# Kernel tuning notes

Measured on AMD Instinct MI355X. Metric: run time of the kernel, lower is better.

## Reference

```python
import jax, jax.numpy as jnp
import numpy as np

_SAMPLING_EPS = 1e-5
B, V = 256, 128000


def _apply_min_p(logits, min_p):
    # probs >= min_p * max_prob  <=>  keep; else logit -> -inf
    probs = jax.nn.softmax(logits, axis=-1)
    max_probs = jnp.max(probs, axis=-1, keepdims=True)
    keep = probs >= (min_p[:, None] * max_probs)
    return jnp.where(keep, logits, -jnp.inf)


def _apply_top_k_top_p(logits, top_k, top_p):
    # Sort ascending once; derive per-row keep-thresholds for both filters.
    logits_sort = jnp.sort(logits, axis=-1)  # [B, V] ascending
    # top-k threshold: value at position V-k (kth largest)
    k_idx = jnp.clip(V - top_k, 0, V - 1).astype(jnp.int32)
    k_thresh = jnp.take_along_axis(logits_sort, k_idx[:, None], axis=-1)  # [B,1]
    # top-p: on ascending-sorted probs, token is kept iff cumsum > 1 - p
    probs_sort = jax.nn.softmax(logits_sort, axis=-1)
    probs_cum = jnp.cumsum(probs_sort, axis=-1)
    kept = probs_cum > (1.0 - top_p[:, None])
    kept = kept.at[:, -1].set(True)  # always keep the max-prob token
    p_thresh = jnp.min(jnp.where(kept, logits_sort, jnp.inf), axis=-1, keepdims=True)
    thresh = jnp.maximum(k_thresh, p_thresh)
    return jnp.where(logits >= thresh, logits, -jnp.inf)


def setup_inputs() -> dict:
    key = jax.random.key(0)
    k1, k2, k3, k4, k5 = jax.random.split(key, 5)
    logits = jax.random.normal(k1, (B, V), jnp.float32)
    temperature = jax.random.uniform(k2, (B,), jnp.float32, 0.1, 1.5)
    temperature = temperature.at[:8].set(0.0)  # greedy rows
    min_p = jax.random.uniform(k3, (B,), jnp.float32, 0.0, 0.2)
    top_k = jax.random.randint(k4, (B,), 1, 64).astype(jnp.int32)
    top_p = jax.random.uniform(k5, (B,), jnp.float32, 0.5, 1.0)
    return {"logits": logits, "temperature": temperature, "min_p": min_p,
            "top_k": top_k, "top_p": top_p}


def reference(logits, temperature, min_p, top_k, top_p):
    logits = logits.astype(jnp.float32)
    greedy = jnp.argmax(logits, axis=-1)  # [B]
    # safe temperature divide (greedy rows have temp ~ 0 but are overridden)
    safe_t = jnp.where(temperature < _SAMPLING_EPS, 1.0, temperature)
    scaled = logits / safe_t[:, None]
    scaled = _apply_min_p(scaled, min_p)
    masked = _apply_top_k_top_p(scaled, top_k, top_p)
    # Gumbel-max trick == categorical sampling from softmax(masked)
    u = jax.random.uniform(jax.random.key(42), masked.shape, jnp.float32, 1e-10, 1.0)
    gumbel = -jnp.log(-jnp.log(u))
    random_sampled = jnp.argmax(masked + gumbel, axis=-1)
    sampled = jnp.where(temperature < _SAMPLING_EPS, greedy, random_sampled)
    return sampled[:, None]  # sampled_token_ids [B, 1]
```

## Files before the change

### kernel.cpp

```cpp
#include <hip/hip_runtime.h>
#include <stdint.h>

typedef unsigned long long u64;
typedef unsigned int u32;

#define VOCAB 128000
#define NV4   32000
#define NROWS 256
#define BLK   1024
#define NW    16
#define NB    4096
#define CAPL  4096
#define SEPS  1e-5f
#define LN2X40 27.725887222397812f

__device__ __forceinline__ u32 f2key(float f){
  u32 u = __float_as_uint(f);
  return (u & 0x80000000u) ? ~u : (u | 0x80000000u);
}
__device__ __forceinline__ float key2f(u32 k){
  u32 u = (k & 0x80000000u) ? (k ^ 0x80000000u) : ~k;
  return __uint_as_float(u);
}

__device__ __forceinline__ void tf2x32(u32 x0, u32 x1, u32 &o0, u32 &o1){
  const u32 k0 = 0u, k1 = 42u, k2 = 0u ^ 42u ^ 0x1BD11BDAu;
  x0 += k0; x1 += k1;
#define TFR(r) { x0 += x1; x1 = (x1 << (r)) | (x1 >> (32 - (r))); x1 ^= x0; }
  TFR(13) TFR(15) TFR(26) TFR(6)
  x0 += k1; x1 += k2 + 1u;
  TFR(17) TFR(29) TFR(16) TFR(24)
  x0 += k2; x1 += k0 + 2u;
  TFR(13) TFR(15) TFR(26) TFR(6)
  x0 += k0; x1 += k1 + 3u;
  TFR(17) TFR(29) TFR(16) TFR(24)
  x0 += k1; x1 += k2 + 4u;
  TFR(13) TFR(15) TFR(26) TFR(6)
  x0 += k2; x1 += k0 + 5u;
#undef TFR
  o0 = x0; o1 = x1;
}
__device__ __forceinline__ u32 gumbel_bits(u32 i){
  u32 o0, o1; tf2x32(0u, i, o0, o1);
  return o0 ^ o1;
}
__device__ __forceinline__ float bits2gumbel(u32 b){
  float f = __uint_as_float(0x3F800000u | (b >> 9)) - 1.0f;
  float u = fmaxf(1e-10f, f + 1e-10f);
  return -logf(-logf(u));
}

__device__ __forceinline__ void cross4096_u32(
    const u32* arr, u32* aux, u32 target, u32* out_idx, u32* out_before, int t)
{
  aux[t] = arr[4*t+0] + arr[4*t+1] + arr[4*t+2] + arr[4*t+3];
  __syncthreads();
  if (t < 64){
    u32 gs = 0u;
    #pragma unroll
    for (int j=0;j<16;j++) gs += aux[t*16+j];
    u32 pref = gs;
    #pragma unroll
    for (int d=1; d<64; d<<=1){ u32 v = __shfl_up(pref, d, 64); if (t >= d) pref += v; }
    u64 bal = __ballot(pref > target);
    int g = bal ? (__ffsll((long long)bal) - 1) : 63;
    u32 pg = __shfl(pref, g, 64);
    u32 gg = __shfl(gs, g, 64);
    if (t == 0){
      u32 c = pg - gg;
      u32 idx = (u32)(g*64 + 63);
      for (int j=0;j<16;j++){
        u32 v = aux[g*16+j];
        if (c + v > target){
          int base = (g*16+j)*4;
          for (int q=0;q<4;q++){
            u32 w = arr[base+q];
            if (c + w > target){ idx = (u32)(base+q); goto doneu; }
            c += w;
          }
        }
        c += v;
      }
      doneu:
      *out_idx = idx; *out_before = c;
    }
  }
}

__device__ __forceinline__ void cross4096_u64(
    const u64* arr, u64* aux, u64 target, u32* out_idx, u64* out_before, int t)
{
  aux[t] = arr[4*t+0] + arr[4*t+1] + arr[4*t+2] + arr[4*t+3];
  __syncthreads();
  if (t < 64){
    u64 gs = 0ull;
    #pragma unroll
    for (int j=0;j<16;j++) gs += aux[t*16+j];
    u64 pref = gs;
    #pragma unroll
    for (int d=1; d<64; d<<=1){
      u64 v = __shfl_up((unsigned long long)pref, d, 64); if (t >= d) pref += v;
    }
    u64 bal = __ballot(pref > target);
    int g = bal ? (__ffsll((long long)bal) - 1) : 63;
    u64 pg = __shfl((unsigned long long)pref, g, 64);
    u64 gg = __shfl((unsigned long long)gs, g, 64);
    if (t == 0){
      u64 c = pg - gg;
      u32 idx = (u32)(g*64 + 63);
      for (int j=0;j<16;j++){
        u64 v = aux[g*16+j];
        if (c + v > target){
          int base = (g*16+j)*4;
          for (int q=0;q<4;q++){
            u64 w = arr[base+q];
            if (c + w > target){ idx = (u32)(base+q); goto donev; }
            c += w;
          }
        }
        c += v;
      }
      donev:
      *out_idx = idx; *out_before = c;
    }
  }
}

__device__ __forceinline__ void cross4096_mass(
    const u64* arr, u64* aux, float topp_v, u64* out_target,
    u32* out_idx, u64* out_before, int t)
{
  aux[t] = arr[4*t+0] + arr[4*t+1] + arr[4*t+2] + arr[4*t+3];
  __syncthreads();
  if (t < 64){
    u64 gs = 0ull;
    #pragma unroll
    for (int j=0;j<16;j++) gs += aux[t*16+j];
    u64 pref = gs;
    #pragma unroll
    for (int d=1; d<64; d<<=1){
      u64 v = __shfl_up((unsigned long long)pref, d, 64); if (t >= d) pref += v;
    }
    u64 total = __shfl((unsigned long long)pref, 63, 64);
    u64 target = (u64)((double)(1.0f - topp_v) * (double)total);
    u64 bal = __ballot(pref > target);
    int g = bal ? (__ffsll((long long)bal) - 1) : 63;
    u64 pg = __shfl((unsigned long long)pref, g, 64);
    u64 gg = __shfl((unsigned long long)gs, g, 64);
    if (t == 0){
      u64 c = pg - gg;
      u32 idx = (u32)(g*64 + 63);
      for (int j=0;j<16;j++){
        u64 v = aux[g*16+j];
        if (c + v > target){
          int base = (g*16+j)*4;
          for (int q=0;q<4;q++){
            u64 w = arr[base+q];
            if (c + w > target){ idx = (u32)(base+q); goto donem; }
            c += w;
          }
        }
        c += v;
      }
      donem:
      *out_target = target; *out_idx = idx; *out_before = c;
    }
  }
}

__device__ __forceinline__ void cross256_u32(const u32* arr, u32 target, u32* out_idx, int t){
  if (t < 64){
    u32 gs = arr[4*t+0]+arr[4*t+1]+arr[4*t+2]+arr[4*t+3];
    u32 pref = gs;
    #pragma unroll
    for (int d=1; d<64; d<<=1){ u32 v=__shfl_up(pref,d,64); if (t>=d) pref+=v; }
    u64 bal = __ballot(pref > target);
    int g = bal ? (__ffsll((long long)bal)-1) : 63;
    u32 pg=__shfl(pref,g,64), gg=__shfl(gs,g,64);
    if (t==0){
      u32 c = pg-gg; u32 idx=(u32)(g*4+3);
      for (int q=0;q<4;q++){ u32 w=arr[g*4+q]; if (c+w>target){ idx=(u32)(g*4+q); break; } c+=w; }
      *out_idx = idx;
    }
  }
}
__device__ __forceinline__ void cross256_u64(const u64* arr, u64 target, u32* out_idx, int t){
  if (t < 64){
    u64 gs = arr[4*t+0]+arr[4*t+1]+arr[4*t+2]+arr[4*t+3];
    u64 pref = gs;
    #pragma unroll
    for (int d=1; d<64; d<<=1){
      u64 v=__shfl_up((unsigned long long)pref,d,64); if (t>=d) pref+=v;
    }
    u64 bal = __ballot(pref > target);
    int g = bal ? (__ffsll((long long)bal)-1) : 63;
    u64 pg=__shfl((unsigned long long)pref,g,64), gg=__shfl((unsigned long long)gs,g,64);
    if (t==0){
      u64 c = pg-gg; u32 idx=(u32)(g*4+3);
      for (int q=0;q<4;q++){ u64 w=arr[g*4+q]; if (c+w>target){ idx=(u32)(g*4+q); break; } c+=w; }
      *out_idx = idx;
    }
  }
}

__device__ __forceinline__ void msmerge(float &m1, float &S1, float m2, float S2){
  float mm = fmaxf(m1, m2);
  if (mm == -INFINITY){ m1 = mm; S1 = 0.0f; return; }
  S1 = S1*__expf(m1-mm) + S2*__expf(m2-mm);
  m1 = mm;
}

__device__ __forceinline__ void argmax_write(
    float best, u32 bi, float* wrf, u32* wru, int ln, int wv, int b, int* out)
{
  #pragma unroll
  for (int d=32; d>0; d>>=1){
    float c2=__shfl_down(best,d,64); u32 i2=__shfl_down(bi,d,64);
    if (c2>best || (c2==best && i2<bi)){best=c2;bi=i2;}
  }
  if (ln==0){ wrf[wv]=best; wru[wv]=bi; }
  __syncthreads();
  if (wv==0){
    float b1=(ln<NW)?wrf[ln]:-INFINITY; u32 i1=(ln<NW)?wru[ln]:0xFFFFFFFFu;
    #pragma unroll
    for (int d=32; d>0; d>>=1){
      float b2=__shfl_down(b1,d,64); u32 i2=__shfl_down(i1,d,64);
      if (b2>b1 || (b2==b1 && i2<i1)){b1=b2;i1=i2;}
    }
    if (ln==0) out[b]=(int)i1;
  }
}

__global__ __launch_bounds__(BLK) void k_all(
    const float* __restrict__ logits, const float* __restrict__ temp,
    const float* __restrict__ minp, const int* __restrict__ topk,
    const float* __restrict__ topp, int* __restrict__ out)
{
  __shared__ u32 cnt[NB];
  __shared__ u64 massI[2*NB];
  __shared__ u64 list[CAPL];
  __shared__ u64 aux64[BLK];
  __shared__ float wrf1[NW], wrf2[NW];
  __shared__ u32  wru1[NW], wru2[NW];
  __shared__ float sh_m, sh_Z;
  __shared__ u32 sh_lstar, sh_len, sh_idx, sh_bef32, sh_u1, sh_u2, sh_u3;
  __shared__ u64 sh_bef64, sh_tfix;

  u32* aux32 = (u32*)aux64;

  const int b = blockIdx.x;
  const int t = threadIdx.x;
  const int ln = t & 63, wv = t >> 6;
  const float T = temp[b];
  const float* row = logits + (size_t)b * VOCAB;
  const float4* row4 = (const float4*)row;

  if (T < SEPS){
    float M = -INFINITY; u32 Mi = 0xFFFFFFFFu;
    for (int i=t; i<NV4; i+=BLK){
      float4 q = row4[i];
      #pragma unroll
      for (int j=0;j<4;j++){
        float l = (&q.x)[j]; u32 gi = (u32)(i*4+j);
        if (l > M){ M = l; Mi = gi; }
      }
    }
    argmax_write(M, Mi, wrf1, wru1, ln, wv, b, out);
    return;
  }

  const float invT = 1.0f / T;
  for (int i=t;i<NB;i+=BLK) cnt[i]=0u;
  for (int i=t;i<2*NB;i+=BLK) massI[i]=0ull;
  if (t==0) sh_len=0u;
  __syncthreads();

  float ms0=-INFINITY,S0=0.0f, ms1=-INFINITY,S1=0.0f,
        ms2=-INFINITY,S2=0.0f, ms3=-INFINITY,S3=0.0f;
#define ONLINE(LV, MS, SS) { \
    float l_ = (LV); \
    atomicAdd(&cnt[f2key(l_)>>20], 1u); \
    float s_ = l_ * invT; \
    float d_ = s_ - MS; \
    float e_ = __expf(-fabsf(d_)); \
    if (d_ > 0.0f){ SS = fmaf(SS, e_, 1.0f); MS = s_; } else { SS += e_; } \
  }
  for (int i=t; i<NV4; i+=2*BLK){
    float4 qa = row4[i];
    int i2 = i + BLK; bool h2 = (i2 < NV4);
    float4 qb; if (h2) qb = row4[i2];
    ONLINE(qa.x,ms0,S0) ONLINE(qa.y,ms1,S1) ONLINE(qa.z,ms2,S2) ONLINE(qa.w,ms3,S3)
    if (h2){
      ONLINE(qb.x,ms0,S0) ONLINE(qb.y,ms1,S1) ONLINE(qb.z,ms2,S2) ONLINE(qb.w,ms3,S3)
    }
  }
#undef ONLINE
  msmerge(ms0,S0,ms1,S1); msmerge(ms2,S2,ms3,S3); msmerge(ms0,S0,ms2,S2);
  #pragma unroll
  for (int d=32; d>0; d>>=1){
    float mz = __shfl_down(ms0, d, 64); float Sz = __shfl_down(S0, d, 64);
    msmerge(ms0, S0, mz, Sz);
  }
  if (ln==0){ wrf1[wv]=ms0; wrf2[wv]=S0; }
  __syncthreads();
  if (wv==0){
    float m1 = (ln<NW)? wrf1[ln] : -INFINITY;
    float Sx = (ln<NW)? wrf2[ln] : 0.0f;
    #pragma unroll
    for (int d=32; d>0; d>>=1){
      float mz=__shfl_down(m1,d,64); float Sz=__shfl_down(Sx,d,64);
      msmerge(m1, Sx, mz, Sz);
    }
    if (ln==0){ sh_m = m1; sh_Z = Sx; }
  }
  __syncthreads();
  const float m = sh_m, Z = sh_Z;

  int tk = topk[b]; if (tk < 1) tk = 1; if (tk > VOCAB) tk = VOCAB;
  cross4096_u32(cnt, aux32, (u32)(VOCAB - tk), &sh_idx, &sh_bef32, t);
  __syncthreads();
  const u32 b1k = sh_idx;
  const u32 r1  = (u32)(VOCAB - tk + 1) - sh_bef32;

  if (wv==0){
    const float rhs = minp[b] * (1.0f / Z);
    u32 lo = 0u, hi = 0xFF800000u;
    while (hi - lo > 64u){
      u32 step = (hi - lo) >> 6;
      u32 k = lo + (u32)(ln + 1) * step;
      float e = __expf(fmaf(key2f(k), invT, -m));
      u64 bal = __ballot((e / Z) >= rhs);
      if (bal){
        u32 g = (u32)(__ffsll((long long)bal) - 1);
        hi = lo + (g + 1u) * step;
        lo = lo + g * step;
      } else {
        lo += 64u * step;
      }
    }
    u32 k = lo + 1u + (u32)ln;
    bool ok = (k <= hi);
    float e = __expf(fmaf(key2f(k), invT, -m));
    u64 bal = __ballot(ok && ((e / Z) >= rhs));
    if (ln==0) sh_lstar = bal ? (lo + 1u + (u32)(__ffsll((long long)bal) - 1)) : hi;
  }
  __syncthreads();
  const u32 lstar = sh_lstar;
  const u32 bl = lstar >> 20;

  {
    u32 pa=0u, pc=0u;
    for (int i=t;i<NB;i+=BLK){
      u32 c = cnt[i];
      if ((u32)i > bl)   pa += c;
      if ((u32)i >= b1k) pc += c;
    }
    #pragma unroll
    for (int d=32; d>0; d>>=1){ pa += __shfl_down(pa,d,64); pc += __shfl_down(pc,d,64); }
    if (ln==0){ wru1[wv]=pa; wru2[wv]=pc; }
    __syncthreads();
    if (t==0){
      u32 a=0u, c2=0u;
      for (int w=0; w<NW; w++){ a += wru1[w]; c2 += wru2[w]; }
      sh_u1 = a; sh_u2 = c2;
    }
    __syncthreads();
  }
  const u32 Kmin = sh_u1;
  const bool kcert = (Kmin >= (u32)tk);
  const u32 CLB = kcert ? b1k : bl;
  const u32 listlen = kcert ? sh_u2 : (Kmin + cnt[bl]);
  const bool fastOK = (listlen <= (u32)CAPL);
  const float cs = LN2X40 - m;

  u32 kc = 0u;
#define P2E(LV, IDX) { \
    float l_ = (LV); u32 key_ = f2key(l_); u32 bk_ = key_ >> 20; \
    if (key_ >= lstar){ \
      kc++; \
      u64 lm_ = (u64)__expf(fmaf(l_, invT, cs)); \
      if (lm_) atomicAdd(&massI[(bk_<<1) | (u32)(t&1)], lm_); \
    } \
    if (fastOK && bk_ >= CLB){ \
      u32 p_ = atomicAdd(&sh_len, 1u); \
      if (p_ < CAPL) list[p_] = ((u64)key_ << 32) | (u64)(u32)(IDX); \
    } \
  }
  for (int i=t; i<NV4; i+=2*BLK){
    float4 qa = row4[i];
    int i2 = i + BLK; bool h2 = (i2 < NV4);
    float4 qb; if (h2) qb = row4[i2];
    P2E(qa.x, i*4+0) P2E(qa.y, i*4+1) P2E(qa.z, i*4+2) P2E(qa.w, i*4+3)
    if (h2){
      P2E(qb.x, i2*4+0) P2E(qb.y, i2*4+1) P2E(qb.z, i2*4+2) P2E(qb.w, i2*4+3)
    }
  }
#undef P2E
  #pragma unroll
  for (int d=32; d>0; d>>=1) kc += __shfl_down(kc, d, 64);
  if (ln==0) wru1[wv] = kc;
  __syncthreads();
  if (t==0){ u32 K2=0u; for (int w=0;w<NW;w++) K2 += wru1[w]; sh_u3 = K2; }
  {
    u64 g0 = massI[8*t+0] + massI[8*t+1];
    u64 g1 = massI[8*t+2] + massI[8*t+3];
    u64 g2 = massI[8*t+4] + massI[8*t+5];
    u64 g3 = massI[8*t+6] + massI[8*t+7];
    __syncthreads();
    massI[4*t+0]=g0; massI[4*t+1]=g1; massI[4*t+2]=g2; massI[4*t+3]=g3;
  }
  __syncthreads();
  const u32 K = sh_u3;
  const bool kval = (K >= (u32)tk);
  const u32 llen = sh_len;

  cross4096_mass(massI, aux64, topp[b], &sh_tfix, &sh_idx, &sh_bef64, t);
  __syncthreads();
  const u32 b1p = sh_idx;
  const u64 t1  = sh_tfix - sh_bef64;
  const bool needK = kval && (b1p <= b1k);
  const bool needP = (!kval) || (b1p >= b1k);

  u32 kkey = 0u, pkey = 0u;

  if (fastOK){
    if (needK){
      for (int i=t;i<NB;i+=BLK) cnt[i]=0u;
      __syncthreads();
      for (u32 i=t; i<llen; i+=BLK){
        u32 key = (u32)(list[i]>>32);
        if ((key>>20) == b1k) atomicAdd(&cnt[(key>>8)&0xFFFu], 1u);
      }
      __syncthreads();
      cross4096_u32(cnt, aux32, r1-1u, &sh_idx, &sh_bef32, t);
      __syncthreads();
      u32 b2k = sh_idx, r2 = r1 - sh_bef32;
      u32 prefk = (b1k<<12) | b2k;
      for (int i=t;i<256;i+=BLK) cnt[i]=0u;
      __syncthreads();
      for (u32 i=t; i<llen; i+=BLK){
        u32 key = (u32)(list[i]>>32);
        if ((key>>8) == prefk) atomicAdd(&cnt[key&0xFFu], 1u);
      }
      __syncthreads();
      cross256_u32(cnt, r2-1u, &sh_idx, t);
      __syncthreads();
      kkey = (prefk<<8) | sh_idx;
    }
    if (needP){
      for (int i=t;i<NB;i+=BLK) massI[i]=0ull;
      __syncthreads();
      for (u32 i=t; i<llen; i+=BLK){
        u32 key = (u32)(list[i]>>32);
        if ((key>>20) == b1p && key >= lstar){
          u64 lm = (u64)__expf(fmaf(key2f(key), invT, cs));
          if (lm) atomicAdd(&massI[(key>>8)&0xFFFu], lm);
        }
      }
      __syncthreads();
      cross4096_u64(massI, aux64, t1, &sh_idx, &sh_bef64, t);
      __syncthreads();
      u32 b2p = sh_idx; u64 t2 = t1 - sh_bef64;
      u32 prefp = (b1p<<12) | b2p;
      for (int i=t;i<256;i+=BLK) massI[i]=0ull;
      __syncthreads();
      for (u32 i=t; i<llen; i+=BLK){
        u32 key = (u32)(list[i]>>32);
        if ((key>>8) == prefp && key >= lstar){
          u64 lm = (u64)__expf(fmaf(key2f(key), invT, cs));
          if (lm) atomicAdd(&massI[key&0xFFu], lm);
        }
      }
      __syncthreads();
      cross256_u64(massI, t2, &sh_idx, t);
      __syncthreads();
      pkey = (prefp<<8) | sh_idx;
    }
    const u32 thrkey = kkey > pkey ? kkey : pkey;

    float best = -INFINITY; u32 bi = 0xFFFFFFFFu;
    for (u32 i=t; i<llen; i+=BLK){
      u64 e = list[i];
      u32 key = (u32)(e>>32);
      if (key >= thrkey){
        u32 idx = (u32)e;
        u32 c = (u32)b * (u32)VOCAB + idx;
        float cand = key2f(key)*invT + bits2gumbel(gumbel_bits(c));
        if (cand > best || (cand == best && idx < bi)){ best = cand; bi = idx; }
      }
    }
    argmax_write(best, bi, wrf1, wru1, ln, wv, b, out);
    return;
  }

  for (int i=t;i<NB;i+=BLK){ cnt[i]=0u; massI[i]=0ull; }
  __syncthreads();
  for (int i=t; i<NV4; i+=BLK){
    float4 q = row4[i];
    #pragma unroll
    for (int j=0;j<4;j++){
      float l = (&q.x)[j]; u32 key = f2key(l); u32 hb = key>>20;
      if (needK && hb == b1k) atomicAdd(&cnt[(key>>8)&0xFFFu], 1u);
      if (needP && hb == b1p && key >= lstar){
        u64 lm = (u64)__expf(fmaf(l, invT, cs));
        if (lm) atomicAdd(&massI[(key>>8)&0xFFFu], lm);
      }
    }
  }
  __syncthreads();
  u32 b2k = 0u, r2 = 1u, b2p = 0u; u64 t2 = 0ull;
  if (needK){
    cross4096_u32(cnt, aux32, r1-1u, &sh_idx, &sh_bef32, t);
    __syncthreads();
    b2k = sh_idx; r2 = r1 - sh_bef32;
  }
  if (needP){
    cross4096_u64(massI, aux64, t1, &sh_idx, &sh_bef64, t);
    __syncthreads();
    b2p = sh_idx; t2 = t1 - sh_bef64;
  }
  const u32 prefk = (b1k<<12) | b2k;
  const u32 prefp = (b1p<<12) | b2p;
  for (int i=t;i<256;i+=BLK){ cnt[i]=0u; massI[i]=0ull; }
  __syncthreads();
  for (int i=t; i<NV4; i+=BLK){
    float4 q = row4[i];
    #pragma unroll
    for (int j=0;j<4;j++){
      float l = (&q.x)[j]; u32 key = f2key(l);
      if (needK && (key>>8) == prefk) atomicAdd(&cnt[key&0xFFu], 1u);
      if (needP && (key>>8) == prefp && key >= lstar){
        u64 lm = (u64)__expf(fmaf(l, invT, cs));
        if (lm) atomicAdd(&massI[key&0xFFu], lm);
      }
    }
  }
  __syncthreads();
  if (needK){
    cross256_u32(cnt, r2-1u, &sh_idx, t);
    __syncthreads();
    kkey = (prefk<<8) | sh_idx;
  }
  if (needP){
    cross256_u64(massI, t2, &sh_idx, t);
    __syncthreads();
    pkey = (prefp<<8) | sh_idx;
  }
  const float thrf = key2f(kkey > pkey ? kkey : pkey);
  float best = -INFINITY; u32 bi = 0xFFFFFFFFu;
  for (int i=t; i<NV4; i+=BLK){
    float4 q = row4[i];
    #pragma unroll
    for (int j=0;j<4;j++){
      float l = (&q.x)[j];
      if (l >= thrf){
        u32 idx = (u32)(i*4+j);
        u32 c = (u32)b * (u32)VOCAB + idx;
        float cand = l*invT + bits2gumbel(gumbel_bits(c));
        if (cand > best || (cand == best && idx < bi)){ best = cand; bi = idx; }
      }
    }
  }
  argmax_write(best, bi, wrf1, wru1, ln, wv, b, out);
}

extern "C" void kernel_launch(void* const* d_in, const int* in_sizes, int n_in,
                              void* d_out, int out_size, void* d_ws, size_t ws_size,
                              hipStream_t stream)
{
  const float* logits = (const float*)d_in[0];
  const float* temp   = (const float*)d_in[1];
  const float* minp   = (const float*)d_in[2];
  const int*   topk   = (const int*)d_in[3];
  const float* topp   = (const float*)d_in[4];
  int* out = (int*)d_out;

  hipLaunchKernelGGL(k_all, dim3(NROWS), dim3(BLK), 0, stream,
                     logits, temp, minp, topk, topp, out);
}
```

Baseline: 60.18 us.

## Privatize histograms per wave group, aggregate list appends, and unroll row loops

```diff
diff --git a/kernel.cpp b/kernel.cpp
--- a/kernel.cpp
+++ b/kernel.cpp
@@ -13,6 +13,7 @@
 #define CAPL  4096
 #define SEPS  1e-5f
 #define LN2X40 27.725887222397812f
+#define MAIN4 28672
 
 __device__ __forceinline__ u32 f2key(float f){
   u32 u = __float_as_uint(f);
@@ -236,8 +237,8 @@
     const float* __restrict__ minp, const int* __restrict__ topk,
     const float* __restrict__ topp, int* __restrict__ out)
 {
-  __shared__ u32 cnt[NB];
-  __shared__ u64 massI[2*NB];
+  __shared__ u32 cnt4[4*NB];
+  __shared__ u64 massI[NB];
   __shared__ u64 list[CAPL];
   __shared__ u64 aux64[BLK];
   __shared__ float wrf1[NW], wrf2[NW];
@@ -247,6 +248,7 @@
   __shared__ u64 sh_bef64, sh_tfix;
 
   u32* aux32 = (u32*)aux64;
+  u32* cnt = cnt4;
 
   const int b = blockIdx.x;
   const int t = threadIdx.x;
@@ -257,42 +259,51 @@
 
   if (T < SEPS){
     float M = -INFINITY; u32 Mi = 0xFFFFFFFFu;
-    for (int i=t; i<NV4; i+=BLK){
-      float4 q = row4[i];
-      #pragma unroll
-      for (int j=0;j<4;j++){
-        float l = (&q.x)[j]; u32 gi = (u32)(i*4+j);
-        if (l > M){ M = l; Mi = gi; }
-      }
-    }
+#define GRE(Q, IDX) { \
+    float l_=(Q); if (l_ > M){ M = l_; Mi = (u32)(IDX); } }
+    for (int i=t; i<MAIN4; i+=4096){
+      float4 q0=row4[i], q1=row4[i+1024], q2=row4[i+2048], q3=row4[i+3072];
+      GRE(q0.x,i*4+0) GRE(q0.y,i*4+1) GRE(q0.z,i*4+2) GRE(q0.w,i*4+3)
+      GRE(q1.x,(i+1024)*4+0) GRE(q1.y,(i+1024)*4+1) GRE(q1.z,(i+1024)*4+2) GRE(q1.w,(i+1024)*4+3)
+      GRE(q2.x,(i+2048)*4+0) GRE(q2.y,(i+2048)*4+1) GRE(q2.z,(i+2048)*4+2) GRE(q2.w,(i+2048)*4+3)
+      GRE(q3.x,(i+3072)*4+0) GRE(q3.y,(i+3072)*4+1) GRE(q3.z,(i+3072)*4+2) GRE(q3.w,(i+3072)*4+3)
+    }
+    for (int i=MAIN4+t; i<NV4; i+=BLK){
+      float4 q=row4[i];
+      GRE(q.x,i*4+0) GRE(q.y,i*4+1) GRE(q.z,i*4+2) GRE(q.w,i*4+3)
+    }
+#undef GRE
     argmax_write(M, Mi, wrf1, wru1, ln, wv, b, out);
     return;
   }
 
   const float invT = 1.0f / T;
-  for (int i=t;i<NB;i+=BLK) cnt[i]=0u;
-  for (int i=t;i<2*NB;i+=BLK) massI[i]=0ull;
+  for (int i=t;i<4*NB;i+=BLK) cnt4[i]=0u;
+  for (int i=t;i<NB;i+=BLK) massI[i]=0ull;
   if (t==0) sh_len=0u;
   __syncthreads();
 
+  u32* mycnt = cnt4 + (((u32)wv & 3u) << 12);
   float ms0=-INFINITY,S0=0.0f, ms1=-INFINITY,S1=0.0f,
         ms2=-INFINITY,S2=0.0f, ms3=-INFINITY,S3=0.0f;
 #define ONLINE(LV, MS, SS) { \
     float l_ = (LV); \
-    atomicAdd(&cnt[f2key(l_)>>20], 1u); \
+    atomicAdd(&mycnt[f2key(l_)>>20], 1u); \
     float s_ = l_ * invT; \
     float d_ = s_ - MS; \
     float e_ = __expf(-fabsf(d_)); \
     if (d_ > 0.0f){ SS = fmaf(SS, e_, 1.0f); MS = s_; } else { SS += e_; } \
   }
-  for (int i=t; i<NV4; i+=2*BLK){
-    float4 qa = row4[i];
-    int i2 = i + BLK; bool h2 = (i2 < NV4);
-    float4 qb; if (h2) qb = row4[i2];
-    ONLINE(qa.x,ms0,S0) ONLINE(qa.y,ms1,S1) ONLINE(qa.z,ms2,S2) ONLINE(qa.w,ms3,S3)
-    if (h2){
-      ONLINE(qb.x,ms0,S0) ONLINE(qb.y,ms1,S1) ONLINE(qb.z,ms2,S2) ONLINE(qb.w,ms3,S3)
-    }
+  for (int i=t; i<MAIN4; i+=4096){
+    float4 q0=row4[i], q1=row4[i+1024], q2=row4[i+2048], q3=row4[i+3072];
+    ONLINE(q0.x,ms0,S0) ONLINE(q0.y,ms1,S1) ONLINE(q0.z,ms2,S2) ONLINE(q0.w,ms3,S3)
+    ONLINE(q1.x,ms0,S0) ONLINE(q1.y,ms1,S1) ONLINE(q1.z,ms2,S2) ONLINE(q1.w,ms3,S3)
+    ONLINE(q2.x,ms0,S0) ONLINE(q2.y,ms1,S1) ONLINE(q2.z,ms2,S2) ONLINE(q2.w,ms3,S3)
+    ONLINE(q3.x,ms0,S0) ONLINE(q3.y,ms1,S1) ONLINE(q3.z,ms2,S2) ONLINE(q3.w,ms3,S3)
+  }
+  for (int i=MAIN4+t; i<NV4; i+=BLK){
+    float4 q=row4[i];
+    ONLINE(q.x,ms0,S0) ONLINE(q.y,ms1,S1) ONLINE(q.z,ms2,S2) ONLINE(q.w,ms3,S3)
   }
 #undef ONLINE
   msmerge(ms0,S0,ms1,S1); msmerge(ms2,S2,ms3,S3); msmerge(ms0,S0,ms2,S2);
@@ -303,6 +314,10 @@
   }
   if (ln==0){ wrf1[wv]=ms0; wrf2[wv]=S0; }
   __syncthreads();
+  for (int i=t; i<NB; i+=BLK){
+    u32 s = cnt4[i] + cnt4[NB+i] + cnt4[2*NB+i] + cnt4[3*NB+i];
+    cnt4[i] = s;
+  }
   if (wv==0){
     float m1 = (ln<NW)? wrf1[ln] : -INFINITY;
     float Sx = (ln<NW)? wrf2[ln] : 0.0f;
@@ -375,25 +390,33 @@
 
   u32 kc = 0u;
 #define P2E(LV, IDX) { \
-    float l_ = (LV); u32 key_ = f2key(l_); u32 bk_ = key_ >> 20; \
+    float l_ = (LV); u32 key_ = f2key(l_); \
     if (key_ >= lstar){ \
       kc++; \
       u64 lm_ = (u64)__expf(fmaf(l_, invT, cs)); \
-      if (lm_) atomicAdd(&massI[(bk_<<1) | (u32)(t&1)], lm_); \
+      if (lm_) atomicAdd(&massI[key_>>20], lm_); \
     } \
-    if (fastOK && bk_ >= CLB){ \
-      u32 p_ = atomicAdd(&sh_len, 1u); \
+    bool cand_ = fastOK && ((key_>>20) >= CLB); \
+    u64 bal_ = __ballot(cand_); \
+    if (cand_){ \
+      u32 lead_ = (u32)__ffsll((long long)bal_) - 1u; \
+      u32 base_ = 0u; \
+      if ((u32)ln == lead_) base_ = atomicAdd(&sh_len, (u32)__popcll(bal_)); \
+      base_ = __shfl(base_, (int)lead_, 64); \
+      u32 p_ = base_ + (u32)__popcll(bal_ & ((1ull << ln) - 1ull)); \
       if (p_ < CAPL) list[p_] = ((u64)key_ << 32) | (u64)(u32)(IDX); \
     } \
   }
-  for (int i=t; i<NV4; i+=2*BLK){
-    float4 qa = row4[i];
-    int i2 = i + BLK; bool h2 = (i2 < NV4);
-    float4 qb; if (h2) qb = row4[i2];
-    P2E(qa.x, i*4+0) P2E(qa.y, i*4+1) P2E(qa.z, i*4+2) P2E(qa.w, i*4+3)
-    if (h2){
-      P2E(qb.x, i2*4+0) P2E(qb.y, i2*4+1) P2E(qb.z, i2*4+2) P2E(qb.w, i2*4+3)
-    }
+  for (int i=t; i<MAIN4; i+=4096){
+    float4 q0=row4[i], q1=row4[i+1024], q2=row4[i+2048], q3=row4[i+3072];
+    P2E(q0.x,i*4+0) P2E(q0.y,i*4+1) P2E(q0.z,i*4+2) P2E(q0.w,i*4+3)
+    P2E(q1.x,(i+1024)*4+0) P2E(q1.y,(i+1024)*4+1) P2E(q1.z,(i+1024)*4+2) P2E(q1.w,(i+1024)*4+3)
+    P2E(q2.x,(i+2048)*4+0) P2E(q2.y,(i+2048)*4+1) P2E(q2.z,(i+2048)*4+2) P2E(q2.w,(i+2048)*4+3)
+    P2E(q3.x,(i+3072)*4+0) P2E(q3.y,(i+3072)*4+1) P2E(q3.z,(i+3072)*4+2) P2E(q3.w,(i+3072)*4+3)
+  }
+  for (int i=MAIN4+t; i<NV4; i+=BLK){
+    float4 q=row4[i];
+    P2E(q.x,i*4+0) P2E(q.y,i*4+1) P2E(q.z,i*4+2) P2E(q.w,i*4+3)
   }
 #undef P2E
   #pragma unroll
@@ -401,14 +424,6 @@
   if (ln==0) wru1[wv] = kc;
   __syncthreads();
   if (t==0){ u32 K2=0u; for (int w=0;w<NW;w++) K2 += wru1[w]; sh_u3 = K2; }
-  {
-    u64 g0 = massI[8*t+0] + massI[8*t+1];
-    u64 g1 = massI[8*t+2] + massI[8*t+3];
-    u64 g2 = massI[8*t+4] + massI[8*t+5];
-    u64 g3 = massI[8*t+6] + massI[8*t+7];
-    __syncthreads();
-    massI[4*t+0]=g0; massI[4*t+1]=g1; massI[4*t+2]=g2; massI[4*t+3]=g3;
-  }
   __syncthreads();
   const u32 K = sh_u3;
   const bool kval = (K >= (u32)tk);
```

Result: no change. 61.18 us (+1.7%).

## Split each row across two cooperative blocks with grid-synchronized merge

Applied to the files above, without the earlier changes.

```diff
diff --git a/kernel.cpp b/kernel.cpp
--- a/kernel.cpp
+++ b/kernel.cpp
@@ -1,18 +1,34 @@
 #include <hip/hip_runtime.h>
+#include <hip/hip_cooperative_groups.h>
 #include <stdint.h>
+
+namespace cg = cooperative_groups;
 
 typedef unsigned long long u64;
 typedef unsigned int u32;
 
 #define VOCAB 128000
 #define NV4   32000
+#define HV4   16000
 #define NROWS 256
 #define BLK   1024
 #define NW    16
 #define NB    4096
-#define CAPL  4096
+#define CAPL  2048
+#define CAPLS 4096
 #define SEPS  1e-5f
 #define LN2X40 27.725887222397812f
+
+#define WS_MASSH   0ull
+#define WS_LIST    16777216ull
+#define WS_CNTH    20971520ull
+#define WS_PARTS   29360128ull
+#define WS_PARTK   29362176ull
+#define WS_PARTGV  29364224ull
+#define WS_PARTGI  29366272ull
+#define WS_LL      29368320ull
+#define WS_KP      29369344ull
+#define WS_NEED    29370368ull
 
 __device__ __forceinline__ u32 f2key(float f){
   u32 u = __float_as_uint(f);
@@ -231,14 +247,400 @@
   }
 }
 
-__global__ __launch_bounds__(BLK) void k_all(
+__global__ __launch_bounds__(BLK, 8) void k_coop(
+    const float* __restrict__ logits, const float* __restrict__ temp,
+    const float* __restrict__ minp, const int* __restrict__ topk,
+    const float* __restrict__ topp, int* __restrict__ out, char* __restrict__ ws)
+{
+  cg::grid_group grid = cg::this_grid();
+
+  __shared__ u32 cnt[NB];
+  __shared__ u64 massI[NB];
+  __shared__ u64 list[CAPL];
+  __shared__ u64 aux64[BLK];
+  __shared__ float wrf1[NW];
+  __shared__ u32  wru1[NW], wru2[NW];
+  __shared__ u32 sh_idx, sh_bef32, sh_lstar, sh_u1, sh_u2;
+  __shared__ u64 sh_bef64, sh_tfix;
+
+  u32* aux32 = (u32*)aux64;
+  u64* massH  = (u64*)(ws + WS_MASSH);
+  u64* wsList = (u64*)(ws + WS_LIST);
+  u32* cntH   = (u32*)(ws + WS_CNTH);
+  float* partS  = (float*)(ws + WS_PARTS);
+  u32*   partK  = (u32*)(ws + WS_PARTK);
+  float* partGV = (float*)(ws + WS_PARTGV);
+  u32*   partGI = (u32*)(ws + WS_PARTGI);
+  u32*   LL     = (u32*)(ws + WS_LL);
+  u32*   KP     = (u32*)(ws + WS_KP);
+
+  const int bid = blockIdx.x;
+  const int r = bid >> 1;
+  const int h = bid & 1;
+  const int t = threadIdx.x;
+  const int ln = t & 63, wv = t >> 6;
+  const float T = temp[r];
+  const bool greedy = (T < SEPS);
+  const float invT = greedy ? 1.0f : (1.0f / T);
+  const float* row = logits + (size_t)r * VOCAB;
+  const float4* row4 = (const float4*)row;
+  const int hb4 = h * HV4, he4 = hb4 + HV4;
+
+  if (t == 0 && h == 0){ LL[r] = 0u; KP[r] = 0u; }
+  if (greedy){
+    float M = -INFINITY; u32 Mi = 0xFFFFFFFFu;
+    for (int i = hb4 + t; i < he4; i += BLK){
+      float4 q = row4[i];
+      #pragma unroll
+      for (int j=0;j<4;j++){
+        float l = (&q.x)[j]; u32 gi = (u32)(i*4+j);
+        if (l > M){ M = l; Mi = gi; }
+      }
+    }
+    #pragma unroll
+    for (int d=32; d>0; d>>=1){
+      float M2=__shfl_down(M,d,64); u32 I2=__shfl_down(Mi,d,64);
+      if (M2>M || (M2==M && I2<Mi)){ M=M2; Mi=I2; }
+    }
+    if (ln==0){ wrf1[wv]=M; wru1[wv]=Mi; }
+    __syncthreads();
+    if (t==0){
+      float b1=wrf1[0]; u32 i1=wru1[0];
+      for (int w=1; w<NW; w++){
+        if (wrf1[w]>b1 || (wrf1[w]==b1 && wru1[w]<i1)){ b1=wrf1[w]; i1=wru1[w]; }
+      }
+      partGV[bid]=b1; partGI[bid]=i1;
+    }
+  } else {
+    for (int i=t;i<NB;i+=BLK) cnt[i]=0u;
+    __syncthreads();
+    u32 km = 0u;
+    float S0=0.0f,S1=0.0f,S2=0.0f,S3=0.0f;
+#define PA(LV, SS) { \
+    float l_=(LV); u32 k_=f2key(l_); \
+    if (k_>km) km=k_; \
+    atomicAdd(&cnt[k_>>20], 1u); \
+    SS += __expf(l_*invT); }
+    for (int i = hb4 + t; i < he4; i += 2*BLK){
+      float4 qa = row4[i];
+      int i2 = i + BLK; bool h2 = (i2 < he4);
+      float4 qb; if (h2) qb = row4[i2];
+      PA(qa.x,S0) PA(qa.y,S1) PA(qa.z,S2) PA(qa.w,S3)
+      if (h2){ PA(qb.x,S0) PA(qb.y,S1) PA(qb.z,S2) PA(qb.w,S3) }
+    }
+#undef PA
+    float S = (S0+S1)+(S2+S3);
+    #pragma unroll
+    for (int d=32; d>0; d>>=1){
+      S += __shfl_down(S,d,64);
+      u32 k2 = __shfl_down(km,d,64); if (k2>km) km=k2;
+    }
+    if (ln==0){ wrf1[wv]=S; wru1[wv]=km; }
+    __syncthreads();
+    for (int i=t;i<NB;i+=BLK) cntH[(size_t)bid*NB + i] = cnt[i];
+    if (t==0){
+      float St=0.0f; u32 kt=0u;
+      for (int w=0; w<NW; w++){ St += wrf1[w]; if (wru1[w]>kt) kt=wru1[w]; }
+      partS[bid]=St; partK[bid]=kt;
+    }
+  }
+  __threadfence();
+  grid.sync();
+
+  float m=0.0f, Z=1.0f, cs=0.0f;
+  u32 b1k=0u, r1=1u, lstar=0u, CLB=0u;
+  int tk=1; bool kcert=false, fastOK=false;
+
+  if (greedy){
+    if (h==0 && t==0){
+      float vA=partGV[bid], vB=partGV[bid+1];
+      u32 iA=partGI[bid], iB=partGI[bid+1];
+      out[r] = (vB>vA || (vB==vA && iB<iA)) ? (int)iB : (int)iA;
+    }
+  } else {
+    const int pb = bid ^ 1;
+    for (int i=t;i<NB;i+=BLK) cnt[i] += cntH[(size_t)pb*NB + i];
+    {
+      u32 kA = partK[bid & ~1], kB = partK[bid | 1];
+      float SA = partS[bid & ~1], SB = partS[bid | 1];
+      u32 kmax = kA > kB ? kA : kB;
+      m = key2f(kmax) * invT;
+      Z = (SA + SB) * __expf(-m);
+    }
+    cs = LN2X40 - m;
+    __syncthreads();
+
+    tk = topk[r]; if (tk < 1) tk = 1; if (tk > VOCAB) tk = VOCAB;
+    cross4096_u32(cnt, aux32, (u32)(VOCAB - tk), &sh_idx, &sh_bef32, t);
+    __syncthreads();
+    b1k = sh_idx;
+    r1  = (u32)(VOCAB - tk + 1) - sh_bef32;
+
+    if (wv==0){
+      const float rhs = minp[r] * (1.0f / Z);
+      u32 lo = 0u, hi = 0xFF800000u;
+      while (hi - lo > 64u){
+        u32 step = (hi - lo) >> 6;
+        u32 k = lo + (u32)(ln + 1) * step;
+        float e = __expf(fmaf(key2f(k), invT, -m));
+        u64 bal = __ballot((e / Z) >= rhs);
+        if (bal){
+          u32 g = (u32)(__ffsll((long long)bal) - 1);
+          hi = lo + (g + 1u) * step;
+          lo = lo + g * step;
+        } else {
+          lo += 64u * step;
+        }
+      }
+      u32 k = lo + 1u + (u32)ln;
+      bool ok = (k <= hi);
+      float e = __expf(fmaf(key2f(k), invT, -m));
+      u64 bal = __ballot(ok && ((e / Z) >= rhs));
+      if (ln==0) sh_lstar = bal ? (lo + 1u + (u32)(__ffsll((long long)bal) - 1)) : hi;
+    }
+    __syncthreads();
+    lstar = sh_lstar;
+    const u32 bl = lstar >> 20;
+
+    {
+      u32 pa=0u, pc=0u;
+      for (int i=t;i<NB;i+=BLK){
+        u32 c = cnt[i];
+        if ((u32)i > bl)   pa += c;
+        if ((u32)i >= b1k) pc += c;
+      }
+      #pragma unroll
+      for (int d=32; d>0; d>>=1){ pa += __shfl_down(pa,d,64); pc += __shfl_down(pc,d,64); }
+      if (ln==0){ wru1[wv]=pa; wru2[wv]=pc; }
+      __syncthreads();
+      if (t==0){
+        u32 a=0u, c2=0u;
+        for (int w=0; w<NW; w++){ a += wru1[w]; c2 += wru2[w]; }
+        sh_u1 = a; sh_u2 = c2;
+      }
+      __syncthreads();
+    }
+    const u32 Kmin = sh_u1;
+    kcert = (Kmin >= (u32)tk);
+    CLB = kcert ? b1k : bl;
+    const u32 listCnt = kcert ? sh_u2 : (Kmin + cnt[bl]);
+    fastOK = (listCnt <= (u32)CAPL);
+  }
+
+  if (!greedy){
+    for (int i=t;i<NB;i+=BLK) massI[i]=0ull;
+    __syncthreads();
+    u32 kc = 0u;
+#define PC(LV, IDX) { \
+    float l_ = (LV); u32 key_ = f2key(l_); \
+    if (key_ >= lstar){ \
+      kc++; \
+      u64 lm_ = (u64)__expf(fmaf(l_, invT, cs)); \
+      if (lm_) atomicAdd(&massI[key_>>20], lm_); \
+    } \
+    bool cand_ = fastOK && ((key_>>20) >= CLB); \
+    u64 bal_ = __ballot(cand_); \
+    if (cand_){ \
+      u32 lead_ = (u32)__ffsll((long long)bal_) - 1u; \
+      u32 base_ = 0u; \
+      if ((u32)ln == lead_) base_ = atomicAdd(&LL[r], (u32)__popcll(bal_)); \
+      base_ = __shfl(base_, (int)lead_, 64); \
+      u32 p_ = base_ + (u32)__popcll(bal_ & ((1ull << ln) - 1ull)); \
+      if (p_ < CAPL) wsList[(size_t)r*CAPL + p_] = ((u64)key_ << 32) | (u64)(u32)(IDX); \
+    } }
+    for (int i = hb4 + t; i < he4; i += 2*BLK){
+      float4 qa = row4[i];
+      int i2 = i + BLK; bool h2 = (i2 < he4);
+      float4 qb; if (h2) qb = row4[i2];
+      PC(qa.x,i*4+0) PC(qa.y,i*4+1) PC(qa.z,i*4+2) PC(qa.w,i*4+3)
+      if (h2){ PC(qb.x,i2*4+0) PC(qb.y,i2*4+1) PC(qb.z,i2*4+2) PC(qb.w,i2*4+3) }
+    }
+#undef PC
+    #pragma unroll
+    for (int d=32; d>0; d>>=1) kc += __shfl_down(kc, d, 64);
+    if (ln==0) wru1[wv] = kc;
+    __syncthreads();
+    if (t==0){
+      u32 K2=0u; for (int w=0;w<NW;w++) K2 += wru1[w];
+      atomicAdd(&KP[r], K2);
+    }
+    if (h==1){
+      for (int i=t;i<NB;i+=BLK) massH[(size_t)bid*NB + i] = massI[i];
+    }
+  }
+  __threadfence();
+  grid.sync();
+
+  if (greedy || h != 0) return;
+
+  for (int i=t;i<NB;i+=BLK) massI[i] += massH[(size_t)(bid+1)*NB + i];
+  __syncthreads();
+  const u32 K = KP[r];
+  const bool kval = (K >= (u32)tk);
+  u32 llen = LL[r]; if (llen > (u32)CAPL) llen = CAPL;
+
+  cross4096_mass(massI, aux64, topp[r], &sh_tfix, &sh_idx, &sh_bef64, t);
+  __syncthreads();
+  const u32 b1p = sh_idx;
+  const u64 t1  = sh_tfix - sh_bef64;
+  const bool needK = kval && (b1p <= b1k);
+  const bool needP = (!kval) || (b1p >= b1k);
+
+  u32 kkey = 0u, pkey = 0u;
+
+  if (fastOK){
+    for (u32 i=t; i<llen; i+=BLK) list[i] = wsList[(size_t)r*CAPL + i];
+    __syncthreads();
+    if (needK){
+      for (int i=t;i<NB;i+=BLK) cnt[i]=0u;
+      __syncthreads();
+      for (u32 i=t; i<llen; i+=BLK){
+        u32 key = (u32)(list[i]>>32);
+        if ((key>>20) == b1k) atomicAdd(&cnt[(key>>8)&0xFFFu], 1u);
+      }
+      __syncthreads();
+      cross4096_u32(cnt, aux32, r1-1u, &sh_idx, &sh_bef32, t);
+      __syncthreads();
+      u32 b2k = sh_idx, r2 = r1 - sh_bef32;
+      u32 prefk = (b1k<<12) | b2k;
+      for (int i=t;i<256;i+=BLK) cnt[i]=0u;
+      __syncthreads();
+      for (u32 i=t; i<llen; i+=BLK){
+        u32 key = (u32)(list[i]>>32);
+        if ((key>>8) == prefk) atomicAdd(&cnt[key&0xFFu], 1u);
+      }
+      __syncthreads();
+      cross256_u32(cnt, r2-1u, &sh_idx, t);
+      __syncthreads();
+      kkey = (prefk<<8) | sh_idx;
+    }
+    if (needP){
+      for (int i=t;i<NB;i+=BLK) massI[i]=0ull;
+      __syncthreads();
+      for (u32 i=t; i<llen; i+=BLK){
+        u32 key = (u32)(list[i]>>32);
+        if ((key>>20) == b1p && key >= lstar){
+          u64 lm = (u64)__expf(fmaf(key2f(key), invT, cs));
+          if (lm) atomicAdd(&massI[(key>>8)&0xFFFu], lm);
+        }
+      }
+      __syncthreads();
+      cross4096_u64(massI, aux64, t1, &sh_idx, &sh_bef64, t);
+      __syncthreads();
+      u32 b2p = sh_idx; u64 t2 = t1 - sh_bef64;
+      u32 prefp = (b1p<<12) | b2p;
+      for (int i=t;i<256;i+=BLK) massI[i]=0ull;
+      __syncthreads();
+      for (u32 i=t; i<llen; i+=BLK){
+        u32 key = (u32)(list[i]>>32);
+        if ((key>>8) == prefp && key >= lstar){
+          u64 lm = (u64)__expf(fmaf(key2f(key), invT, cs));
+          if (lm) atomicAdd(&massI[key&0xFFu], lm);
+        }
+      }
+      __syncthreads();
+      cross256_u64(massI, t2, &sh_idx, t);
+      __syncthreads();
+      pkey = (prefp<<8) | sh_idx;
+    }
+    const u32 thrkey = kkey > pkey ? kkey : pkey;
+
+    float best = -INFINITY; u32 bi = 0xFFFFFFFFu;
+    for (u32 i=t; i<llen; i+=BLK){
+      u64 e = list[i];
+      u32 key = (u32)(e>>32);
+      if (key >= thrkey){
+        u32 idx = (u32)e;
+        u32 c = (u32)r * (u32)VOCAB + idx;
+        float cand = key2f(key)*invT + bits2gumbel(gumbel_bits(c));
+        if (cand > best || (cand == best && idx < bi)){ best = cand; bi = idx; }
+      }
+    }
+    argmax_write(best, bi, wrf1, wru1, ln, wv, r, out);
+    return;
+  }
+
+  for (int i=t;i<NB;i+=BLK) cnt[i]=0u;
+  { __syncthreads(); }
+  for (int i=t;i<NB;i+=BLK) massI[i]=0ull;
+  __syncthreads();
+  for (int i=t; i<NV4; i+=BLK){
+    float4 q = row4[i];
+    #pragma unroll
+    for (int j=0;j<4;j++){
+      float l = (&q.x)[j]; u32 key = f2key(l); u32 hb = key>>20;
+      if (needK && hb == b1k) atomicAdd(&cnt[(key>>8)&0xFFFu], 1u);
+      if (needP && hb == b1p && key >= lstar){
+        u64 lm = (u64)__expf(fmaf(l, invT, cs));
+        if (lm) atomicAdd(&massI[(key>>8)&0xFFFu], lm);
+      }
+    }
+  }
+  __syncthreads();
+  u32 b2k = 0u, r2 = 1u, b2p = 0u; u64 t2 = 0ull;
+  if (needK){
+    cross4096_u32(cnt, aux32, r1-1u, &sh_idx, &sh_bef32, t);
+    __syncthreads();
+    b2k = sh_idx; r2 = r1 - sh_bef32;
+  }
+  if (needP){
+    cross4096_u64(massI, aux64, t1, &sh_idx, &sh_bef64, t);
+    __syncthreads();
+    b2p = sh_idx; t2 = t1 - sh_bef64;
+  }
+  const u32 prefk = (b1k<<12) | b2k;
+  const u32 prefp = (b1p<<12) | b2p;
+  for (int i=t;i<256;i+=BLK){ cnt[i]=0u; massI[i]=0ull; }
+  __syncthreads();
+  for (int i=t; i<NV4; i+=BLK){
+    float4 q = row4[i];
+    #pragma unroll
+    for (int j=0;j<4;j++){
+      float l = (&q.x)[j]; u32 key = f2key(l);
+      if (needK && (key>>8) == prefk) atomicAdd(&cnt[key&0xFFu], 1u);
+      if (needP && (key>>8) == prefp && key >= lstar){
+        u64 lm = (u64)__expf(fmaf(l, invT, cs));
+        if (lm) atomicAdd(&massI[key&0xFFu], lm);
+      }
+    }
+  }
+  __syncthreads();
+  if (needK){
+    cross256_u32(cnt, r2-1u, &sh_idx, t);
+    __syncthreads();
+    kkey = (prefk<<8) | sh_idx;
+  }
+  if (needP){
+    cross256_u64(massI, t2, &sh_idx, t);
+    __syncthreads();
+    pkey = (prefp<<8) | sh_idx;
+  }
+  const float thrf = key2f(kkey > pkey ? kkey : pkey);
+  float best = -INFINITY; u32 bi = 0xFFFFFFFFu;
+  for (int i=t; i<NV4; i+=BLK){
+    float4 q = row4[i];
+    #pragma unroll
+    for (int j=0;j<4;j++){
+      float l = (&q.x)[j];
+      if (l >= thrf){
+        u32 idx = (u32)(i*4+j);
+        u32 c = (u32)r * (u32)VOCAB + idx;
+        float cand = l*invT + bits2gumbel(gumbel_bits(c));
+        if (cand > best || (cand == best && idx < bi)){ best = cand; bi = idx; }
+      }
+    }
+  }
+  argmax_write(best, bi, wrf1, wru1, ln, wv, r, out);
+}
+
+__global__ __launch_bounds__(BLK) void k_single(
     const float* __restrict__ logits, const float* __restrict__ temp,
     const float* __restrict__ minp, const int* __restrict__ topk,
     const float* __restrict__ topp, int* __restrict__ out)
 {
   __shared__ u32 cnt[NB];
-  __shared__ u64 massI[2*NB];
-  __shared__ u64 list[CAPL];
+  __shared__ u64 massI[NB];
+  __shared__ u64 list[CAPLS];
   __shared__ u64 aux64[BLK];
   __shared__ float wrf1[NW], wrf2[NW];
   __shared__ u32  wru1[NW], wru2[NW];
@@ -270,8 +672,7 @@
   }
 
   const float invT = 1.0f / T;
-  for (int i=t;i<NB;i+=BLK) cnt[i]=0u;
-  for (int i=t;i<2*NB;i+=BLK) massI[i]=0ull;
+  for (int i=t;i<NB;i+=BLK){ cnt[i]=0u; massI[i]=0ull; }
   if (t==0) sh_len=0u;
   __syncthreads();
 
@@ -370,20 +771,20 @@
   const bool kcert = (Kmin >= (u32)tk);
   const u32 CLB = kcert ? b1k : bl;
   const u32 listlen = kcert ? sh_u2 : (Kmin + cnt[bl]);
-  const bool fastOK = (listlen <= (u32)CAPL);
+  const bool fastOK = (listlen <= (u32)CAPLS);
   const float cs = LN2X40 - m;
 
   u32 kc = 0u;
 #define P2E(LV, IDX) { \
-    float l_ = (LV); u32 key_ = f2key(l_); u32 bk_ = key_ >> 20; \
+    float l_ = (LV); u32 key_ = f2key(l_); \
     if (key_ >= lstar){ \
       kc++; \
       u64 lm_ = (u64)__expf(fmaf(l_, invT, cs)); \
-      if (lm_) atomicAdd(&massI[(bk_<<1) | (u32)(t&1)], lm_); \
+      if (lm_) atomicAdd(&massI[key_>>20], lm_); \
     } \
-    if (fastOK && bk_ >= CLB){ \
+    if (fastOK && (key_>>20) >= CLB){ \
       u32 p_ = atomicAdd(&sh_len, 1u); \
-      if (p_ < CAPL) list[p_] = ((u64)key_ << 32) | (u64)(u32)(IDX); \
+      if (p_ < CAPLS) list[p_] = ((u64)key_ << 32) | (u64)(u32)(IDX); \
     } \
   }
   for (int i=t; i<NV4; i+=2*BLK){
@@ -401,14 +802,6 @@
   if (ln==0) wru1[wv] = kc;
   __syncthreads();
   if (t==0){ u32 K2=0u; for (int w=0;w<NW;w++) K2 += wru1[w]; sh_u3 = K2; }
-  {
-    u64 g0 = massI[8*t+0] + massI[8*t+1];
-    u64 g1 = massI[8*t+2] + massI[8*t+3];
-    u64 g2 = massI[8*t+4] + massI[8*t+5];
-    u64 g3 = massI[8*t+6] + massI[8*t+7];
-    __syncthreads();
-    massI[4*t+0]=g0; massI[4*t+1]=g1; massI[4*t+2]=g2; massI[4*t+3]=g3;
-  }
   __syncthreads();
   const u32 K = sh_u3;
   const bool kval = (K >= (u32)tk);
@@ -574,7 +967,18 @@
   const int*   topk   = (const int*)d_in[3];
   const float* topp   = (const float*)d_in[4];
   int* out = (int*)d_out;
-
-  hipLaunchKernelGGL(k_all, dim3(NROWS), dim3(BLK), 0, stream,
-                     logits, temp, minp, topk, topp, out);
-}
+  char* ws = (char*)d_ws;
+
+  int maxb = 0;
+  hipError_t oe = hipOccupancyMaxActiveBlocksPerMultiprocessor(&maxb, k_coop, BLK, 0);
+  const bool coop_ok = (ws_size >= (size_t)WS_NEED) && (oe == hipSuccess) && (maxb >= 2);
+
+  if (coop_ok){
+    void* args[] = { (void*)&logits, (void*)&temp, (void*)&minp, (void*)&topk,
+                     (void*)&topp, (void*)&out, (void*)&ws };
+    hipLaunchCooperativeKernel(k_coop, dim3(2*NROWS), dim3(BLK), args, 0, stream);
+  } else {
+    hipLaunchKernelGGL(k_single, dim3(NROWS), dim3(BLK), 0, stream,
+                       logits, temp, minp, topk, topp, out);
+  }
+}
```

Result: no change. 59.40 us (-1.3%).
